# Performance work log

Measured on AMD Instinct MI355X. Metric: run time of the kernel, lower is better.

## Reference

```python
import jax, jax.numpy as jnp
import numpy as np

B, X, H, R, M = 256, 512, 1024, 512, 512
F_BIAS = 1.0

def setup_inputs() -> dict:
    key = jax.random.key(0)
    ks = jax.random.split(key, 8)
    s = lambda fan: 1.0 / np.sqrt(fan)
    return {
        "x": jax.random.normal(ks[0], (B, X), jnp.float32),
        "h": jax.random.normal(ks[1], (B, H), jnp.float32),
        "c": jnp.tanh(jax.random.normal(ks[2], (B, H), jnp.float32)),
        "hmem": jax.random.normal(ks[3], (B, M, R), jnp.float32),
        "W_full": jax.random.normal(ks[4], (X + R + H, R + 4 * H), jnp.float32) * s(X + R + H),
        "bias": jnp.zeros((R + 4 * H,), jnp.float32),
        "W_full1": jax.random.normal(ks[5], (X + R + H, R + H), jnp.float32) * s(X + R + H),
        "bias1": jnp.zeros((R + H,), jnp.float32),
        "trans_w": jax.random.normal(ks[6], (R, X + H), jnp.float32) * s(X + H),
        "trans_b": jnp.zeros((R,), jnp.float32),
        "fc_w": jax.random.normal(ks[7], (M, X + H), jnp.float32) * s(X + H),
        "fc_b": jnp.zeros((M,), jnp.float32),
    }

def reference(x, h, c, hmem, W_full, bias, W_full1, bias1, trans_w, trans_b, fc_w, fc_b):
    h_size = H
    # soft read head over memory slots
    read_head = jnp.concatenate([x, c], axis=1) @ fc_w.T + fc_b          # [B, M]
    h_index = jax.nn.softmax(read_head, axis=1)                          # [B, M]
    h_entry = jnp.einsum('bm,bmr->br', h_index, hmem)                    # [B, R]
    # gated double-projection
    concat = jnp.concatenate([x, c, h_entry], axis=1)                    # [B, X+H+R]
    g = jax.nn.sigmoid(concat @ W_full1 + bias1)                         # [B, R+H]
    gate = jnp.concatenate([jnp.ones_like(x), g], axis=1)                # [B, X+H+R]
    pre = (concat * gate) @ W_full + bias                                # [B, R+4H]
    i = pre[:, 0*h_size:1*h_size]
    j = pre[:, 1*h_size:2*h_size]
    f = pre[:, 2*h_size:3*h_size]
    o = pre[:, 3*h_size:4*h_size]
    om = pre[:, 4*h_size:]                                               # [B, R]
    new_c = jnp.tanh(c * jax.nn.sigmoid(f + F_BIAS) + jax.nn.sigmoid(i) * jnp.tanh(j))
    new_h = new_c * jax.nn.sigmoid(o)
    r_out = h_entry * jax.nn.sigmoid(om)
    # steady-state write: soft index (detached), broadcast overwrite
    w_index = jax.lax.stop_gradient(h_index)                             # [B, M]
    w_val = jnp.concatenate([x, new_c], axis=1) @ trans_w.T + trans_b    # [B, R]
    new_hmem = w_val[:, None, :] * w_index[:, :, None] + hmem * (1.0 - w_index[:, :, None])
    new_r = jnp.concatenate([new_h, r_out], axis=1)                      # [B, H+R]
    return new_r, new_h, new_c, new_hmem
```

## Files before the change

kernel.cpp:

```cpp
#include <hip/hip_runtime.h>
#include <hip/hip_bf16.h>
#include <cstddef>

#define BB 256
#define XX 512
#define HH 1024
#define RR 512
#define MM 512
#define KCAT 2048
#define KXC 1536
#define NFULL 4608
#define NG 1536

#define OFF_NH (BB*1536)
#define OFF_NC (OFF_NH + BB*HH)
#define OFF_HM (OFF_NC + BB*HH)

typedef __attribute__((ext_vector_type(8))) short bf16x8;
typedef __attribute__((ext_vector_type(4))) short s16x4;
typedef __attribute__((ext_vector_type(4))) float f32x4;

__device__ __forceinline__ float sigm(float x) { return 1.0f / (1.0f + expf(-x)); }

__device__ __forceinline__ unsigned short f2bf(float f) {
    unsigned u = __float_as_uint(f);
    u = u + 0x7fffu + ((u >> 16) & 1u);
    return (unsigned short)(u >> 16);
}
__device__ __forceinline__ float bf2f(unsigned short h) {
    return __uint_as_float((unsigned)h << 16);
}


__global__ __launch_bounds__(256) void convw_k(const float* __restrict__ src,
                                               short* __restrict__ hi,
                                               short* __restrict__ lo) {
    size_t e0 = ((size_t)blockIdx.x * 256 + threadIdx.x) * 8;
    short hs[8], ls[8];
    #pragma unroll
    for (int q = 0; q < 2; ++q) {
        float4 v = reinterpret_cast<const float4*>(src + e0)[q];
        float f[4] = {v.x, v.y, v.z, v.w};
        #pragma unroll
        for (int e = 0; e < 4; ++e) {
            unsigned short hb = f2bf(f[e]);
            hs[q * 4 + e] = (short)hb;
            ls[q * 4 + e] = (short)f2bf(f[e] - bf2f(hb));
        }
    }
    *reinterpret_cast<bf16x8*>(hi + e0) = *reinterpret_cast<bf16x8*>(&hs[0]);
    *reinterpret_cast<bf16x8*>(lo + e0) = *reinterpret_cast<bf16x8*>(&ls[0]);
}

__global__ __launch_bounds__(256) void convt_k(const float* __restrict__ W0,
                                               short* __restrict__ T0hi, short* __restrict__ T0lo,
                                               const float* __restrict__ W1,
                                               short* __restrict__ T1hi, short* __restrict__ T1lo) {
    __shared__ __align__(16) short lh[64][72];
    __shared__ __align__(16) short ll[64][72];
    const int tid = threadIdx.x;
    const int by = blockIdx.y;
    const float* W;
    short *Thi, *Tlo;
    int Ndim, n0;
    if (by < 72) { W = W0; Thi = T0hi; Tlo = T0lo; Ndim = NFULL; n0 = by * 64; }
    else         { W = W1; Thi = T1hi; Tlo = T1lo; Ndim = NG;    n0 = (by - 72) * 64; }
    const int k0 = blockIdx.x * 64;
    {
        int kr = (tid >> 4) * 4;
        int nc = (tid & 15) * 4;
        #pragma unroll
        for (int i = 0; i < 4; ++i) {
            float4 v = *reinterpret_cast<const float4*>(W + (size_t)(k0 + kr + i) * Ndim + n0 + nc);
            float f[4] = {v.x, v.y, v.z, v.w};
            #pragma unroll
            for (int e = 0; e < 4; ++e) {
                unsigned short hb = f2bf(f[e]);
                lh[nc + e][kr + i] = (short)hb;
                ll[nc + e][kr + i] = (short)f2bf(f[e] - bf2f(hb));
            }
        }
    }
    __syncthreads();
    {
        int nl = tid >> 2;
        int kq = (tid & 3) * 16;
        size_t base = (size_t)(n0 + nl) * KCAT + k0 + kq;
        *reinterpret_cast<bf16x8*>(Thi + base)     = *reinterpret_cast<const bf16x8*>(&lh[nl][kq]);
        *reinterpret_cast<bf16x8*>(Thi + base + 8) = *reinterpret_cast<const bf16x8*>(&lh[nl][kq + 8]);
        *reinterpret_cast<bf16x8*>(Tlo + base)     = *reinterpret_cast<const bf16x8*>(&ll[nl][kq]);
        *reinterpret_cast<bf16x8*>(Tlo + base + 8) = *reinterpret_cast<const bf16x8*>(&ll[nl][kq + 8]);
    }
}

__global__ __launch_bounds__(256) void prep_k(const float* __restrict__ x,
                                              const float* __restrict__ c,
                                              short* __restrict__ cat_hi,
                                              short* __restrict__ cat_lo) {
    int i = blockIdx.x * 256 + threadIdx.x;
    int e0 = i * 4;
    int b = e0 / KXC, q = e0 - b * KXC;
    float4 v = (q < XX) ? *reinterpret_cast<const float4*>(x + (size_t)b * XX + q)
                        : *reinterpret_cast<const float4*>(c + (size_t)b * HH + (q - XX));
    float f[4] = {v.x, v.y, v.z, v.w};
    s16x4 hv, lv;
    #pragma unroll
    for (int e = 0; e < 4; ++e) {
        unsigned short hb = f2bf(f[e]);
        hv[e] = (short)hb;
        lv[e] = (short)f2bf(f[e] - bf2f(hb));
    }
    *reinterpret_cast<s16x4*>(cat_hi + (size_t)b * KCAT + q) = hv;
    *reinterpret_cast<s16x4*>(cat_lo + (size_t)b * KCAT + q) = lv;
}

template<int GATHER>
__global__ __launch_bounds__(256, 2) void mgemm_k(const short* __restrict__ A0h,
                                                  const short* __restrict__ A0l, int lda0,
                                                  const short* __restrict__ A1h,
                                                  const short* __restrict__ A1l, int lda1,
                                                  const short* __restrict__ Bh_,
                                                  const short* __restrict__ Bl_, int ldb,
                                                  const float* __restrict__ bias,
                                                  float* __restrict__ Cbase, int ldc,
                                                  size_t chunk_stride, int kchunk) {
    __shared__ __align__(16) short Ah[64][72];
    __shared__ __align__(16) short Al[64][72];
    __shared__ __align__(16) short Bh[128][72];
    __shared__ __align__(16) short Bl[128][72];

    const int tid = threadIdx.x;
    const int col0 = blockIdx.x * 128;
    const int row0 = blockIdx.y * 64;
    const int z = blockIdx.z;
    const int kbeg = z * kchunk;
    float* C = Cbase + (size_t)z * chunk_stride;

    const int lane = tid & 63, w = tid >> 6;
    const int rm = (w >> 1) * 32, cn = (w & 1) * 64;
    const int fr = lane & 15, kg = lane >> 4;

    const int ar = tid >> 2, akq = (tid & 3) * 16;
    const int br = tid >> 1, bkq = (tid & 1) * 32;

    f32x4 acc[2][4] = {};
    int4 pa[4], pb[8];

    const short* bHrow = Bh_ + (size_t)(col0 + br) * ldb + bkq;
    const short* bLrow = Bl_ + (size_t)(col0 + br) * ldb + bkq;

    const int steps = kchunk >> 6;

    {
        int gk = kbeg + akq;
        const short* ah_ = (GATHER && gk >= XX) ? A1h + (size_t)(row0 + ar) * lda1 + (gk - XX)
                                                : A0h + (size_t)(row0 + ar) * lda0 + gk;
        const short* al_ = (GATHER && gk >= XX) ? A1l + (size_t)(row0 + ar) * lda1 + (gk - XX)
                                                : A0l + (size_t)(row0 + ar) * lda0 + gk;
        pa[0] = *reinterpret_cast<const int4*>(ah_);
        pa[1] = *reinterpret_cast<const int4*>(ah_ + 8);
        pa[2] = *reinterpret_cast<const int4*>(al_);
        pa[3] = *reinterpret_cast<const int4*>(al_ + 8);
        #pragma unroll
        for (int j = 0; j < 4; ++j) {
            pb[j]     = *reinterpret_cast<const int4*>(bHrow + kbeg + j * 8);
            pb[4 + j] = *reinterpret_cast<const int4*>(bLrow + kbeg + j * 8);
        }
    }

    for (int t = 0; t < steps; ++t) {
        *reinterpret_cast<int4*>(&Ah[ar][akq])     = pa[0];
        *reinterpret_cast<int4*>(&Ah[ar][akq + 8]) = pa[1];
        *reinterpret_cast<int4*>(&Al[ar][akq])     = pa[2];
        *reinterpret_cast<int4*>(&Al[ar][akq + 8]) = pa[3];
        #pragma unroll
        for (int j = 0; j < 4; ++j) {
            *reinterpret_cast<int4*>(&Bh[br][bkq + j * 8]) = pb[j];
            *reinterpret_cast<int4*>(&Bl[br][bkq + j * 8]) = pb[4 + j];
        }
        __syncthreads();
        if (t + 1 < steps) {
            int kc = kbeg + (t + 1) * 64;
            int gk = kc + akq;
            const short* ah_ = (GATHER && gk >= XX) ? A1h + (size_t)(row0 + ar) * lda1 + (gk - XX)
                                                    : A0h + (size_t)(row0 + ar) * lda0 + gk;
            const short* al_ = (GATHER && gk >= XX) ? A1l + (size_t)(row0 + ar) * lda1 + (gk - XX)
                                                    : A0l + (size_t)(row0 + ar) * lda0 + gk;
            pa[0] = *reinterpret_cast<const int4*>(ah_);
            pa[1] = *reinterpret_cast<const int4*>(ah_ + 8);
            pa[2] = *reinterpret_cast<const int4*>(al_);
            pa[3] = *reinterpret_cast<const int4*>(al_ + 8);
            #pragma unroll
            for (int j = 0; j < 4; ++j) {
                pb[j]     = *reinterpret_cast<const int4*>(bHrow + kc + j * 8);
                pb[4 + j] = *reinterpret_cast<const int4*>(bLrow + kc + j * 8);
            }
        }
        #pragma unroll
        for (int ks = 0; ks < 64; ks += 32) {
            bf16x8 ah2[2], al2[2], bh4[4], bl4[4];
            #pragma unroll
            for (int mf = 0; mf < 2; ++mf) {
                ah2[mf] = *reinterpret_cast<const bf16x8*>(&Ah[rm + mf * 16 + fr][ks + kg * 8]);
                al2[mf] = *reinterpret_cast<const bf16x8*>(&Al[rm + mf * 16 + fr][ks + kg * 8]);
            }
            #pragma unroll
            for (int nf = 0; nf < 4; ++nf) {
                bh4[nf] = *reinterpret_cast<const bf16x8*>(&Bh[cn + nf * 16 + fr][ks + kg * 8]);
                bl4[nf] = *reinterpret_cast<const bf16x8*>(&Bl[cn + nf * 16 + fr][ks + kg * 8]);
            }
            #pragma unroll
            for (int mf = 0; mf < 2; ++mf)
                #pragma unroll
                for (int nf = 0; nf < 4; ++nf) {
                    acc[mf][nf] = __builtin_amdgcn_mfma_f32_16x16x32_bf16(ah2[mf], bh4[nf], acc[mf][nf], 0, 0, 0);
                    acc[mf][nf] = __builtin_amdgcn_mfma_f32_16x16x32_bf16(ah2[mf], bl4[nf], acc[mf][nf], 0, 0, 0);
                    acc[mf][nf] = __builtin_amdgcn_mfma_f32_16x16x32_bf16(al2[mf], bh4[nf], acc[mf][nf], 0, 0, 0);
                }
        }
        __syncthreads();
    }

    #pragma unroll
    for (int mf = 0; mf < 2; ++mf)
        #pragma unroll
        for (int nf = 0; nf < 4; ++nf)
            #pragma unroll
            for (int i = 0; i < 4; ++i) {
                int row = row0 + rm + mf * 16 + kg * 4 + i;
                int col = col0 + cn + nf * 16 + fr;
                float v = acc[mf][nf][i];
                if (z == 0) v += bias[col];
                C[(size_t)row * ldc + col] = v;
            }
}

__global__ __launch_bounds__(512) void smax_k(const float* __restrict__ rhp,
                                              float* __restrict__ hidx) {
    __shared__ float red[8];
    __shared__ float red2[8];
    int b = blockIdx.x, t = threadIdx.x;
    float v = 0.f;
    #pragma unroll
    for (int zz = 0; zz < 6; ++zz) v += rhp[(size_t)zz * (BB * MM) + (size_t)b * MM + t];
    float m = v;
    #pragma unroll
    for (int off = 1; off < 64; off <<= 1) m = fmaxf(m, __shfl_xor(m, off));
    int wid = t >> 6, lane = t & 63;
    if (lane == 0) red[wid] = m;
    __syncthreads();
    float mm = red[0];
    #pragma unroll
    for (int i = 1; i < 8; ++i) mm = fmaxf(mm, red[i]);
    float e = expf(v - mm);
    float s = e;
    #pragma unroll
    for (int off = 1; off < 64; off <<= 1) s += __shfl_xor(s, off);
    if (lane == 0) red2[wid] = s;
    __syncthreads();
    float tot = red2[0];
    #pragma unroll
    for (int i = 1; i < 8; ++i) tot += red2[i];
    hidx[(size_t)b * MM + t] = e / tot;
}

__global__ __launch_bounds__(512) void hepart_k(const float* __restrict__ hidx,
                                                const float* __restrict__ hmem,
                                                float* __restrict__ hep) {
    __shared__ float wi[128];
    int b = blockIdx.x, s = blockIdx.y, t = threadIdx.x;
    if (t < 128) wi[t] = hidx[(size_t)b * MM + s * 128 + t];
    __syncthreads();
    const float* hm = hmem + ((size_t)b * MM + (size_t)s * 128) * RR + t;
    float acc = 0.f;
    #pragma unroll 8
    for (int j = 0; j < 128; ++j) acc += wi[j] * hm[(size_t)j * RR];
    hep[((size_t)s * BB + b) * RR + t] = acc;
}

__global__ __launch_bounds__(256) void hefin_k(const float* __restrict__ hep,
                                               short* __restrict__ cat_hi,
                                               short* __restrict__ cat_lo) {
    int i = blockIdx.x * 256 + threadIdx.x;
    int b = i >> 9, r = i & (RR - 1);
    float acc = 0.f;
    #pragma unroll
    for (int s = 0; s < 4; ++s) acc += hep[((size_t)s * BB + b) * RR + r];
    size_t base = (size_t)b * KCAT + KXC + r;
    unsigned short hb = f2bf(acc);
    cat_hi[base] = (short)hb;
    cat_lo[base] = (short)f2bf(acc - bf2f(hb));
}

__global__ __launch_bounds__(256) void gfin_k(const float* __restrict__ gp,
                                              const short* __restrict__ cat_hi,
                                              const short* __restrict__ cat_lo,
                                              short* __restrict__ gatg_hi,
                                              short* __restrict__ gatg_lo) {
    int i = blockIdx.x * 256 + threadIdx.x;
    int b = i / NG, q = i - b * NG;
    float s = 0.f;
    #pragma unroll
    for (int zz = 0; zz < 4; ++zz) s += gp[(size_t)zz * (BB * NG) + (size_t)b * NG + q];
    size_t base = (size_t)b * KCAT + XX + q;
    float e = bf2f((unsigned short)cat_hi[base]) + bf2f((unsigned short)cat_lo[base]);
    float gv = e * sigm(s);
    unsigned short hb = f2bf(gv);
    gatg_hi[(size_t)b * NG + q] = (short)hb;
    gatg_lo[(size_t)b * NG + q] = (short)f2bf(gv - bf2f(hb));
}

__global__ __launch_bounds__(256) void lstm_k(const float* __restrict__ pre0,
                                              const float* __restrict__ c,
                                              const short* __restrict__ cat_hi,
                                              const short* __restrict__ cat_lo,
                                              float* __restrict__ out,
                                              short* __restrict__ ncg_hi,
                                              short* __restrict__ ncg_lo) {
    const float* pre1 = pre0 + (size_t)BB * NFULL;
    int idx = blockIdx.x * 256 + threadIdx.x;
    int b = idx / 1536, q = idx - b * 1536;
    size_t pb = (size_t)b * NFULL;
    if (q < HH) {
        float iv = pre0[pb + q] + pre1[pb + q];
        float jv = pre0[pb + HH + q] + pre1[pb + HH + q];
        float fv = pre0[pb + 2 * HH + q] + pre1[pb + 2 * HH + q];
        float ov = pre0[pb + 3 * HH + q] + pre1[pb + 3 * HH + q];
        float cc = c[(size_t)b * HH + q];
        float nc = tanhf(cc * sigm(fv + 1.0f) + sigm(iv) * tanhf(jv));
        float nh = nc * sigm(ov);
        out[(size_t)b * 1536 + q] = nh;
        out[OFF_NH + (size_t)b * HH + q] = nh;
        out[OFF_NC + (size_t)b * HH + q] = nc;
        unsigned short hb = f2bf(nc);
        ncg_hi[(size_t)b * HH + q] = (short)hb;
        ncg_lo[(size_t)b * HH + q] = (short)f2bf(nc - bf2f(hb));
    } else {
        int r = q - HH;
        float om = pre0[pb + 4 * HH + r] + pre1[pb + 4 * HH + r];
        size_t base = (size_t)b * KCAT + KXC + r;
        float he = bf2f((unsigned short)cat_hi[base]) + bf2f((unsigned short)cat_lo[base]);
        out[(size_t)b * 1536 + HH + r] = he * sigm(om);
    }
}

__global__ __launch_bounds__(256) void wvred_k(const float* __restrict__ wvp,
                                               float* __restrict__ wval) {
    int i = blockIdx.x * 256 + threadIdx.x;
    size_t e = (size_t)i * 4;
    float4 acc = {0.f, 0.f, 0.f, 0.f};
    #pragma unroll
    for (int zz = 0; zz < 6; ++zz) {
        float4 p = *reinterpret_cast<const float4*>(wvp + (size_t)zz * (BB * RR) + e);
        acc.x += p.x; acc.y += p.y; acc.z += p.z; acc.w += p.w;
    }
    *reinterpret_cast<float4*>(wval + e) = acc;
}

__global__ __launch_bounds__(256) void hmemupd_k(const float* __restrict__ hmem,
                                                 const float* __restrict__ wval,
                                                 const float* __restrict__ widx,
                                                 float* __restrict__ outhm) {
    size_t n4 = (size_t)BB * MM * RR / 4;
    size_t stride = (size_t)gridDim.x * blockDim.x;
    for (size_t i = (size_t)blockIdx.x * blockDim.x + threadIdx.x; i < n4; i += stride) {
        size_t e = i * 4;
        int r = (int)(e & (RR - 1));
        int m = (int)((e >> 9) & (MM - 1));
        int b = (int)(e >> 18);
        float wi = widx[(size_t)b * MM + m];
        float om = 1.0f - wi;
        float4 hv = *reinterpret_cast<const float4*>(hmem + e);
        float4 wv = *reinterpret_cast<const float4*>(wval + (size_t)b * RR + r);
        float4 o;
        o.x = wv.x * wi + hv.x * om;
        o.y = wv.y * wi + hv.y * om;
        o.z = wv.z * wi + hv.z * om;
        o.w = wv.w * wi + hv.w * om;
        *reinterpret_cast<float4*>(outhm + e) = o;
    }
}


__global__ __launch_bounds__(256) void prep3_k(const float* __restrict__ x,
                                               const float* __restrict__ c,
                                               float* __restrict__ concatb,
                                               float* __restrict__ gated) {
    int idx = blockIdx.x * 256 + threadIdx.x;
    int b = idx / KXC, q = idx - b * KXC;
    float v;
    if (q < XX) { v = x[b * XX + q]; gated[(size_t)b * KCAT + q] = v; }
    else v = c[b * HH + (q - XX)];
    concatb[(size_t)b * KCAT + q] = v;
}

template<int AMODE, int BLAYOUT, int EPI>
__global__ __launch_bounds__(256) void mgemm3_k(const float* __restrict__ A0,
                                                const float* __restrict__ A1,
                                                const float* __restrict__ W,
                                                const float* __restrict__ bias,
                                                float* __restrict__ C,
                                                const float* __restrict__ E,
                                                int N, int K) {
    __shared__ __align__(16) short Ah[64][72];
    __shared__ __align__(16) short Al[64][72];
    __shared__ __align__(16) short Bh[64][72];
    __shared__ __align__(16) short Bl[64][72];
    const int tid = threadIdx.x;
    const int row0 = blockIdx.y * 64, col0 = blockIdx.x * 64;
    const int lane = tid & 63, w = tid >> 6;
    const int rm = (w >> 1) * 32, cn = (w & 1) * 32;
    const int fr = lane & 15, kg = lane >> 4;
    const int ar = tid >> 2, akq = (tid & 3) * 16;
    const int bkk = (tid >> 4) * 4, bnn = (tid & 15) * 4;
    f32x4 acc[2][2] = {};
    for (int k0 = 0; k0 < K; k0 += 64) {
        {
            const float* src;
            if (AMODE == 0) src = A0 + (size_t)(row0 + ar) * K + k0 + akq;
            else {
                int gk = k0 + akq;
                src = (gk < XX) ? (A0 + (size_t)(row0 + ar) * XX + gk)
                                : (A1 + (size_t)(row0 + ar) * HH + (gk - XX));
            }
            short hs[16], ls[16];
            #pragma unroll
            for (int q = 0; q < 4; ++q) {
                float4 v = reinterpret_cast<const float4*>(src)[q];
                float f[4] = {v.x, v.y, v.z, v.w};
                #pragma unroll
                for (int e = 0; e < 4; ++e) {
                    unsigned short hb = f2bf(f[e]);
                    hs[q * 4 + e] = (short)hb;
                    ls[q * 4 + e] = (short)f2bf(f[e] - bf2f(hb));
                }
            }
            *reinterpret_cast<bf16x8*>(&Ah[ar][akq])     = *reinterpret_cast<bf16x8*>(&hs[0]);
            *reinterpret_cast<bf16x8*>(&Ah[ar][akq + 8]) = *reinterpret_cast<bf16x8*>(&hs[8]);
            *reinterpret_cast<bf16x8*>(&Al[ar][akq])     = *reinterpret_cast<bf16x8*>(&ls[0]);
            *reinterpret_cast<bf16x8*>(&Al[ar][akq + 8]) = *reinterpret_cast<bf16x8*>(&ls[8]);
        }
        if (BLAYOUT == 1) {
            const float* src = W + (size_t)(col0 + ar) * K + k0 + akq;
            short hs[16], ls[16];
            #pragma unroll
            for (int q = 0; q < 4; ++q) {
                float4 v = reinterpret_cast<const float4*>(src)[q];
                float f[4] = {v.x, v.y, v.z, v.w};
                #pragma unroll
                for (int e = 0; e < 4; ++e) {
                    unsigned short hb = f2bf(f[e]);
                    hs[q * 4 + e] = (short)hb;
                    ls[q * 4 + e] = (short)f2bf(f[e] - bf2f(hb));
                }
            }
            *reinterpret_cast<bf16x8*>(&Bh[ar][akq])     = *reinterpret_cast<bf16x8*>(&hs[0]);
            *reinterpret_cast<bf16x8*>(&Bh[ar][akq + 8]) = *reinterpret_cast<bf16x8*>(&hs[8]);
            *reinterpret_cast<bf16x8*>(&Bl[ar][akq])     = *reinterpret_cast<bf16x8*>(&ls[0]);
            *reinterpret_cast<bf16x8*>(&Bl[ar][akq + 8]) = *reinterpret_cast<bf16x8*>(&ls[8]);
        } else {
            float4 r0 = *reinterpret_cast<const float4*>(W + (size_t)(k0 + bkk + 0) * N + col0 + bnn);
            float4 r1 = *reinterpret_cast<const float4*>(W + (size_t)(k0 + bkk + 1) * N + col0 + bnn);
            float4 r2 = *reinterpret_cast<const float4*>(W + (size_t)(k0 + bkk + 2) * N + col0 + bnn);
            float4 r3 = *reinterpret_cast<const float4*>(W + (size_t)(k0 + bkk + 3) * N + col0 + bnn);
            float col[4][4] = {{r0.x, r1.x, r2.x, r3.x}, {r0.y, r1.y, r2.y, r3.y},
                               {r0.z, r1.z, r2.z, r3.z}, {r0.w, r1.w, r2.w, r3.w}};
            #pragma unroll
            for (int j = 0; j < 4; ++j) {
                s16x4 hv, lv;
                #pragma unroll
                for (int e = 0; e < 4; ++e) {
                    unsigned short hb = f2bf(col[j][e]);
                    hv[e] = (short)hb;
                    lv[e] = (short)f2bf(col[j][e] - bf2f(hb));
                }
                *reinterpret_cast<s16x4*>(&Bh[bnn + j][bkk]) = hv;
                *reinterpret_cast<s16x4*>(&Bl[bnn + j][bkk]) = lv;
            }
        }
        __syncthreads();
        #pragma unroll
        for (int ks = 0; ks < 64; ks += 32) {
            bf16x8 ah[2], al[2], bh[2], bl[2];
            #pragma unroll
            for (int mf = 0; mf < 2; ++mf) {
                ah[mf] = *reinterpret_cast<const bf16x8*>(&Ah[rm + mf * 16 + fr][ks + kg * 8]);
                al[mf] = *reinterpret_cast<const bf16x8*>(&Al[rm + mf * 16 + fr][ks + kg * 8]);
            }
            #pragma unroll
            for (int nf = 0; nf < 2; ++nf) {
                bh[nf] = *reinterpret_cast<const bf16x8*>(&Bh[cn + nf * 16 + fr][ks + kg * 8]);
                bl[nf] = *reinterpret_cast<const bf16x8*>(&Bl[cn + nf * 16 + fr][ks + kg * 8]);
            }
            #pragma unroll
            for (int mf = 0; mf < 2; ++mf)
                #pragma unroll
                for (int nf = 0; nf < 2; ++nf) {
                    acc[mf][nf] = __builtin_amdgcn_mfma_f32_16x16x32_bf16(ah[mf], bh[nf], acc[mf][nf], 0, 0, 0);
                    acc[mf][nf] = __builtin_amdgcn_mfma_f32_16x16x32_bf16(ah[mf], bl[nf], acc[mf][nf], 0, 0, 0);
                    acc[mf][nf] = __builtin_amdgcn_mfma_f32_16x16x32_bf16(al[mf], bh[nf], acc[mf][nf], 0, 0, 0);
                }
        }
        __syncthreads();
    }
    #pragma unroll
    for (int mf = 0; mf < 2; ++mf)
        #pragma unroll
        for (int nf = 0; nf < 2; ++nf)
            #pragma unroll
            for (int i = 0; i < 4; ++i) {
                int row = row0 + rm + mf * 16 + kg * 4 + i;
                int col = col0 + cn + nf * 16 + fr;
                float v = acc[mf][nf][i] + bias[col];
                if (EPI == 0) C[(size_t)row * N + col] = v;
                else {
                    size_t base = (size_t)row * KCAT + XX + col;
                    C[base] = E[base] * sigm(v);
                }
            }
}

__global__ __launch_bounds__(256) void softmax3_k(float* __restrict__ rh) {
    int b = blockIdx.x;
    float* row = rh + (size_t)b * MM;
    int t = threadIdx.x;
    float v0 = row[t], v1 = row[t + 256];
    float m = fmaxf(v0, v1);
    #pragma unroll
    for (int off = 1; off < 64; off <<= 1) m = fmaxf(m, __shfl_xor(m, off));
    __shared__ float red[8];
    int wid = t >> 6, lane = t & 63;
    if (lane == 0) red[wid] = m;
    __syncthreads();
    float mm = fmaxf(fmaxf(red[0], red[1]), fmaxf(red[2], red[3]));
    float e0 = expf(v0 - mm), e1 = expf(v1 - mm);
    float s = e0 + e1;
    #pragma unroll
    for (int off = 1; off < 64; off <<= 1) s += __shfl_xor(s, off);
    if (lane == 0) red[4 + wid] = s;
    __syncthreads();
    float inv = 1.0f / (red[4] + red[5] + red[6] + red[7]);
    row[t] = e0 * inv;
    row[t + 256] = e1 * inv;
}

__global__ __launch_bounds__(512) void hentry3_k(const float* __restrict__ hidx,
                                                 const float* __restrict__ hmem,
                                                 float* __restrict__ concatb) {
    int b = blockIdx.x;
    int r = threadIdx.x;
    __shared__ float wi[MM];
    wi[r] = hidx[(size_t)b * MM + r];
    __syncthreads();
    const float* hm = hmem + (size_t)b * MM * RR + r;
    float acc = 0.f;
    #pragma unroll 8
    for (int m = 0; m < MM; ++m) acc += wi[m] * hm[(size_t)m * RR];
    concatb[(size_t)b * KCAT + KXC + r] = acc;
}

__global__ __launch_bounds__(256) void lstm3_k(const float* __restrict__ pre,
                                               const float* __restrict__ c,
                                               const float* __restrict__ concatb,
                                               float* __restrict__ out) {
    int idx = blockIdx.x * 256 + threadIdx.x;
    int b = idx / 1536, q = idx - b * 1536;
    const float* p = pre + (size_t)b * NFULL;
    if (q < HH) {
        float iv = p[q], jv = p[HH + q], fv = p[2 * HH + q], ov = p[3 * HH + q];
        float cc = c[(size_t)b * HH + q];
        float nc = tanhf(cc * sigm(fv + 1.0f) + sigm(iv) * tanhf(jv));
        float nh = nc * sigm(ov);
        out[(size_t)b * 1536 + q] = nh;
        out[OFF_NH + (size_t)b * HH + q] = nh;
        out[OFF_NC + (size_t)b * HH + q] = nc;
    } else {
        int r = q - HH;
        float om = p[4 * HH + r];
        float he = concatb[(size_t)b * KCAT + KXC + r];
        out[(size_t)b * 1536 + HH + r] = he * sigm(om);
    }
}

extern "C" void kernel_launch(void* const* d_in, const int* in_sizes, int n_in,
                              void* d_out, int out_size, void* d_ws, size_t ws_size,
                              hipStream_t stream) {
    const float* x      = (const float*)d_in[0];
    const float* c      = (const float*)d_in[2];
    const float* hmem   = (const float*)d_in[3];
    const float* W_full = (const float*)d_in[4];
    const float* bias   = (const float*)d_in[5];
    const float* W_full1= (const float*)d_in[6];
    const float* bias1  = (const float*)d_in[7];
    const float* trans_w= (const float*)d_in[8];
    const float* trans_b= (const float*)d_in[9];
    const float* fc_w   = (const float*)d_in[10];
    const float* fc_b   = (const float*)d_in[11];

    float* out = (float*)d_out;

    constexpr size_t SZ_WT    = (size_t)NFULL * KCAT * 2;
    constexpr size_t SZ_WT1   = (size_t)NG * KCAT * 2;
    constexpr size_t SZ_FCW   = (size_t)MM * KXC * 2;
    constexpr size_t SZ_CAT   = (size_t)BB * KCAT * 2;
    constexpr size_t SZ_GATG  = (size_t)BB * NG * 2;
    constexpr size_t SZ_NCG   = (size_t)BB * HH * 2;
    constexpr size_t SZ_HIDX  = (size_t)BB * MM * 4;
    constexpr size_t SZ_RH6   = 6 * (size_t)BB * MM * 4;
    constexpr size_t SZ_HEP   = 4 * (size_t)BB * RR * 4;
    constexpr size_t SZ_GP4   = 4 * (size_t)BB * NG * 4;
    constexpr size_t SZ_PRE2  = 2 * (size_t)BB * NFULL * 4;
    constexpr size_t SZ_WV6   = 6 * (size_t)BB * RR * 4;
    constexpr size_t SZ_WVAL  = (size_t)BB * RR * 4;
    constexpr size_t SZ_WT1R  = 2 * SZ_WT1;
    constexpr size_t SZ_FWR   = 2 * SZ_FCW;
    constexpr size_t SZ_G1    = SZ_PRE2;
    constexpr size_t NEED = 2 * SZ_WT + SZ_WT1R + SZ_FWR + 2 * SZ_CAT
                          + 2 * SZ_GATG + 2 * SZ_NCG + SZ_HIDX + SZ_G1;

    if (ws_size >= NEED) {
        char* p = (char*)d_ws;
        short* wt_hi   = (short*)p; p += SZ_WT;
        short* wt_lo   = (short*)p; p += SZ_WT;
        char*  wt1r    = p;         p += SZ_WT1R;
        char*  fwr     = p;         p += SZ_FWR;
        short* cat_hi  = (short*)p; p += SZ_CAT;
        short* cat_lo  = (short*)p; p += SZ_CAT;
        short* gatg_hi = (short*)p; p += SZ_GATG;
        short* gatg_lo = (short*)p; p += SZ_GATG;
        short* ncg_hi  = (short*)p; p += SZ_NCG;
        short* ncg_lo  = (short*)p; p += SZ_NCG;
        float* hidx    = (float*)p; p += SZ_HIDX;
        char*  g1      = p;

        short* wt1_hi = (short*)wt1r;
        short* wt1_lo = (short*)(wt1r + SZ_WT1);
        float* wv6    = (float*)wt1r;
        float* wval   = (float*)(wt1r + SZ_WV6);
        short* fcw_hi = (short*)fwr;
        short* fcw_lo = (short*)(fwr + SZ_FCW);
        short* trw_hi = (short*)fwr;
        short* trw_lo = (short*)(fwr + SZ_FCW);
        float* rh6    = (float*)g1;
        float* hep    = (float*)g1;
        float* gp4    = (float*)g1;
        float* pre2   = (float*)g1;

        convt_k<<<dim3(KCAT / 64, 96), 256, 0, stream>>>(W_full, wt_hi, wt_lo,
                                                         W_full1, wt1_hi, wt1_lo);
        convw_k<<<MM * KXC / 8 / 256, 256, 0, stream>>>(fc_w, fcw_hi, fcw_lo);
        prep_k<<<BB * KXC / 4 / 256, 256, 0, stream>>>(x, c, cat_hi, cat_lo);
        mgemm_k<0><<<dim3(MM / 128, BB / 64, 6), 256, 0, stream>>>(
            cat_hi, cat_lo, KCAT, nullptr, nullptr, 0,
            fcw_hi, fcw_lo, KXC, fc_b, rh6, MM, (size_t)BB * MM, KXC / 6);
        smax_k<<<BB, 512, 0, stream>>>(rh6, hidx);
        hepart_k<<<dim3(BB, 4), 512, 0, stream>>>(hidx, hmem, hep);
        hefin_k<<<BB * RR / 256, 256, 0, stream>>>(hep, cat_hi, cat_lo);
        mgemm_k<0><<<dim3(NG / 128, BB / 64, 4), 256, 0, stream>>>(
            cat_hi, cat_lo, KCAT, nullptr, nullptr, 0,
            wt1_hi, wt1_lo, KCAT, bias1, gp4, NG, (size_t)BB * NG, KCAT / 4);
        gfin_k<<<BB * NG / 256, 256, 0, stream>>>(gp4, cat_hi, cat_lo, gatg_hi, gatg_lo);
        mgemm_k<1><<<dim3(NFULL / 128, BB / 64, 2), 256, 0, stream>>>(
            cat_hi, cat_lo, KCAT, gatg_hi, gatg_lo, NG,
            wt_hi, wt_lo, KCAT, bias, pre2, NFULL, (size_t)BB * NFULL, KCAT / 2);
        lstm_k<<<BB * 1536 / 256, 256, 0, stream>>>(pre2, c, cat_hi, cat_lo,
                                                    out, ncg_hi, ncg_lo);
        convw_k<<<RR * KXC / 8 / 256, 256, 0, stream>>>(trans_w, trw_hi, trw_lo);
        mgemm_k<1><<<dim3(RR / 128, BB / 64, 6), 256, 0, stream>>>(
            cat_hi, cat_lo, KCAT, ncg_hi, ncg_lo, HH,
            trw_hi, trw_lo, KXC, trans_b, wv6, RR, (size_t)BB * RR, KXC / 6);
        wvred_k<<<BB * RR / 4 / 256, 256, 0, stream>>>(wv6, wval);
        hmemupd_k<<<4096, 256, 0, stream>>>(hmem, wval, hidx, out + OFF_HM);
    } else {
        float* ws      = (float*)d_ws;
        float* hidx    = ws;
        float* concatb = hidx + BB * MM;
        float* gated   = concatb + BB * KCAT;
        float* pre     = gated + BB * KCAT;
        float* wval    = pre + BB * NFULL;
        float* new_c   = out + OFF_NC;

        prep3_k<<<BB * KXC / 256, 256, 0, stream>>>(x, c, concatb, gated);
        mgemm3_k<1, 1, 0><<<dim3(MM / 64, BB / 64), 256, 0, stream>>>(
            x, c, fc_w, fc_b, hidx, nullptr, MM, KXC);
        softmax3_k<<<BB, 256, 0, stream>>>(hidx);
        hentry3_k<<<BB, 512, 0, stream>>>(hidx, hmem, concatb);
        mgemm3_k<0, 0, 1><<<dim3(NG / 64, BB / 64), 256, 0, stream>>>(
            concatb, nullptr, W_full1, bias1, gated, concatb, NG, KCAT);
        mgemm3_k<0, 0, 0><<<dim3(NFULL / 64, BB / 64), 256, 0, stream>>>(
            gated, nullptr, W_full, bias, pre, nullptr, NFULL, KCAT);
        lstm3_k<<<BB * 1536 / 256, 256, 0, stream>>>(pre, c, concatb, out);
        mgemm3_k<1, 1, 0><<<dim3(RR / 64, BB / 64), 256, 0, stream>>>(
            x, new_c, trans_w, trans_b, wval, nullptr, RR, KXC);
        hmemupd_k<<<4096, 256, 0, stream>>>(hmem, wval, hidx, out + OFF_HM);
    }
}
```

Baseline: 402.0 us.

## Enlarge GEMM tiles to 128x128 with swizzled LDS and fuse partial reduction into hmem update

The split-bf16 MFMA GEMM now uses 128x128 output tiles, with each wave computing a 64x64 sub-tile. Shared memory is unpadded and XOR-swizzled to avoid bank conflicts, and the K-split count for the narrow GEMMs is doubled to 12 to keep enough blocks. The separate wvred reduction kernel is removed, and the hmem update kernel now sums the 12 partials per batch row in shared memory before streaming the memory update. The larger tiles raise reuse per LDS load but cut the block count and raise register pressure. The extra K-splits also mean more partial traffic.

```diff
diff --git a/kernel.cpp b/kernel.cpp
--- a/kernel.cpp
+++ b/kernel.cpp
@@ -124,105 +124,116 @@
                                                   const float* __restrict__ bias,
                                                   float* __restrict__ Cbase, int ldc,
                                                   size_t chunk_stride, int kchunk) {
-    __shared__ __align__(16) short Ah[64][72];
-    __shared__ __align__(16) short Al[64][72];
-    __shared__ __align__(16) short Bh[128][72];
-    __shared__ __align__(16) short Bl[128][72];
+    __shared__ __align__(16) short Ah[128 * 64];
+    __shared__ __align__(16) short Al[128 * 64];
+    __shared__ __align__(16) short Bh[128 * 64];
+    __shared__ __align__(16) short Bl[128 * 64];
 
     const int tid = threadIdx.x;
-    const int col0 = blockIdx.x * 128;
-    const int row0 = blockIdx.y * 64;
+    const int col0 = blockIdx.x * 128, row0 = blockIdx.y * 128;
     const int z = blockIdx.z;
     const int kbeg = z * kchunk;
     float* C = Cbase + (size_t)z * chunk_stride;
 
     const int lane = tid & 63, w = tid >> 6;
-    const int rm = (w >> 1) * 32, cn = (w & 1) * 64;
+    const int rm = (w >> 1) * 64, cn = (w & 1) * 64;
     const int fr = lane & 15, kg = lane >> 4;
 
-    const int ar = tid >> 2, akq = (tid & 3) * 16;
-    const int br = tid >> 1, bkq = (tid & 1) * 32;
-
-    f32x4 acc[2][4] = {};
-    int4 pa[4], pb[8];
-
-    const short* bHrow = Bh_ + (size_t)(col0 + br) * ldb + bkq;
-    const short* bLrow = Bl_ + (size_t)(col0 + br) * ldb + bkq;
+    const int sr = tid >> 1;
+    const int so = (tid & 1) * 64;
+    const int sks = so >> 1;
+    const int swr = (sr & 7) << 4;
+
+    f32x4 acc[4][4] = {};
+    int4 pa[8], pb[8];
 
     const int steps = kchunk >> 6;
 
-    {
-        int gk = kbeg + akq;
-        const short* ah_ = (GATHER && gk >= XX) ? A1h + (size_t)(row0 + ar) * lda1 + (gk - XX)
-                                                : A0h + (size_t)(row0 + ar) * lda0 + gk;
-        const short* al_ = (GATHER && gk >= XX) ? A1l + (size_t)(row0 + ar) * lda1 + (gk - XX)
-                                                : A0l + (size_t)(row0 + ar) * lda0 + gk;
-        pa[0] = *reinterpret_cast<const int4*>(ah_);
-        pa[1] = *reinterpret_cast<const int4*>(ah_ + 8);
-        pa[2] = *reinterpret_cast<const int4*>(al_);
-        pa[3] = *reinterpret_cast<const int4*>(al_ + 8);
+    #define LOADA(GK0)                                                           \
+        {   int gk = (GK0) + sks;                                                \
+            const short *ah_, *al_;                                              \
+            if (GATHER && gk >= XX) {                                            \
+                ah_ = A1h + (size_t)(row0 + sr) * lda1 + (gk - XX);              \
+                al_ = A1l + (size_t)(row0 + sr) * lda1 + (gk - XX);              \
+            } else {                                                             \
+                ah_ = A0h + (size_t)(row0 + sr) * lda0 + gk;                     \
+                al_ = A0l + (size_t)(row0 + sr) * lda0 + gk;                     \
+            }                                                                    \
+            pa[0] = *reinterpret_cast<const int4*>(ah_);                         \
+            pa[1] = *reinterpret_cast<const int4*>(ah_ + 8);                     \
+            pa[2] = *reinterpret_cast<const int4*>(ah_ + 16);                    \
+            pa[3] = *reinterpret_cast<const int4*>(ah_ + 24);                    \
+            pa[4] = *reinterpret_cast<const int4*>(al_);                         \
+            pa[5] = *reinterpret_cast<const int4*>(al_ + 8);                     \
+            pa[6] = *reinterpret_cast<const int4*>(al_ + 16);                    \
+            pa[7] = *reinterpret_cast<const int4*>(al_ + 24);                    \
+        }
+    #define LOADB(GK0)                                                           \
+        {   const short* bh_ = Bh_ + (size_t)(col0 + sr) * ldb + (GK0) + sks;    \
+            const short* bl_ = Bl_ + (size_t)(col0 + sr) * ldb + (GK0) + sks;    \
+            pb[0] = *reinterpret_cast<const int4*>(bh_);                         \
+            pb[1] = *reinterpret_cast<const int4*>(bh_ + 8);                     \
+            pb[2] = *reinterpret_cast<const int4*>(bh_ + 16);                    \
+            pb[3] = *reinterpret_cast<const int4*>(bh_ + 24);                    \
+            pb[4] = *reinterpret_cast<const int4*>(bl_);                         \
+            pb[5] = *reinterpret_cast<const int4*>(bl_ + 8);                     \
+            pb[6] = *reinterpret_cast<const int4*>(bl_ + 16);                    \
+            pb[7] = *reinterpret_cast<const int4*>(bl_ + 24);                    \
+        }
+
+    LOADA(kbeg)
+    LOADB(kbeg)
+
+    char* aH = (char*)Ah + sr * 128;
+    char* aL = (char*)Al + sr * 128;
+    char* bH = (char*)Bh + sr * 128;
+    char* bL = (char*)Bl + sr * 128;
+
+    for (int t = 0; t < steps; ++t) {
         #pragma unroll
         for (int j = 0; j < 4; ++j) {
-            pb[j]     = *reinterpret_cast<const int4*>(bHrow + kbeg + j * 8);
-            pb[4 + j] = *reinterpret_cast<const int4*>(bLrow + kbeg + j * 8);
-        }
-    }
-
-    for (int t = 0; t < steps; ++t) {
-        *reinterpret_cast<int4*>(&Ah[ar][akq])     = pa[0];
-        *reinterpret_cast<int4*>(&Ah[ar][akq + 8]) = pa[1];
-        *reinterpret_cast<int4*>(&Al[ar][akq])     = pa[2];
-        *reinterpret_cast<int4*>(&Al[ar][akq + 8]) = pa[3];
-        #pragma unroll
-        for (int j = 0; j < 4; ++j) {
-            *reinterpret_cast<int4*>(&Bh[br][bkq + j * 8]) = pb[j];
-            *reinterpret_cast<int4*>(&Bl[br][bkq + j * 8]) = pb[4 + j];
+            int off = (so + j * 16) ^ swr;
+            *reinterpret_cast<int4*>(aH + off) = pa[j];
+            *reinterpret_cast<int4*>(aL + off) = pa[4 + j];
+            *reinterpret_cast<int4*>(bH + off) = pb[j];
+            *reinterpret_cast<int4*>(bL + off) = pb[4 + j];
         }
         __syncthreads();
         if (t + 1 < steps) {
             int kc = kbeg + (t + 1) * 64;
-            int gk = kc + akq;
-            const short* ah_ = (GATHER && gk >= XX) ? A1h + (size_t)(row0 + ar) * lda1 + (gk - XX)
-                                                    : A0h + (size_t)(row0 + ar) * lda0 + gk;
-            const short* al_ = (GATHER && gk >= XX) ? A1l + (size_t)(row0 + ar) * lda1 + (gk - XX)
-                                                    : A0l + (size_t)(row0 + ar) * lda0 + gk;
-            pa[0] = *reinterpret_cast<const int4*>(ah_);
-            pa[1] = *reinterpret_cast<const int4*>(ah_ + 8);
-            pa[2] = *reinterpret_cast<const int4*>(al_);
-            pa[3] = *reinterpret_cast<const int4*>(al_ + 8);
-            #pragma unroll
-            for (int j = 0; j < 4; ++j) {
-                pb[j]     = *reinterpret_cast<const int4*>(bHrow + kc + j * 8);
-                pb[4 + j] = *reinterpret_cast<const int4*>(bLrow + kc + j * 8);
-            }
+            LOADA(kc)
+            LOADB(kc)
         }
         #pragma unroll
-        for (int ks = 0; ks < 64; ks += 32) {
-            bf16x8 ah2[2], al2[2], bh4[4], bl4[4];
-            #pragma unroll
-            for (int mf = 0; mf < 2; ++mf) {
-                ah2[mf] = *reinterpret_cast<const bf16x8*>(&Ah[rm + mf * 16 + fr][ks + kg * 8]);
-                al2[mf] = *reinterpret_cast<const bf16x8*>(&Al[rm + mf * 16 + fr][ks + kg * 8]);
+        for (int ksi = 0; ksi < 2; ++ksi) {
+            int fro = (ksi * 64 + kg * 16) ^ ((fr & 7) << 4);
+            bf16x8 ah4[4], al4[4];
+            #pragma unroll
+            for (int mf = 0; mf < 4; ++mf) {
+                int row = rm + mf * 16 + fr;
+                ah4[mf] = *reinterpret_cast<const bf16x8*>((char*)Ah + row * 128 + fro);
+                al4[mf] = *reinterpret_cast<const bf16x8*>((char*)Al + row * 128 + fro);
             }
             #pragma unroll
             for (int nf = 0; nf < 4; ++nf) {
-                bh4[nf] = *reinterpret_cast<const bf16x8*>(&Bh[cn + nf * 16 + fr][ks + kg * 8]);
-                bl4[nf] = *reinterpret_cast<const bf16x8*>(&Bl[cn + nf * 16 + fr][ks + kg * 8]);
-            }
-            #pragma unroll
-            for (int mf = 0; mf < 2; ++mf)
+                int col = cn + nf * 16 + fr;
+                bf16x8 bh8 = *reinterpret_cast<const bf16x8*>((char*)Bh + col * 128 + fro);
+                bf16x8 bl8 = *reinterpret_cast<const bf16x8*>((char*)Bl + col * 128 + fro);
                 #pragma unroll
-                for (int nf = 0; nf < 4; ++nf) {
-                    acc[mf][nf] = __builtin_amdgcn_mfma_f32_16x16x32_bf16(ah2[mf], bh4[nf], acc[mf][nf], 0, 0, 0);
-                    acc[mf][nf] = __builtin_amdgcn_mfma_f32_16x16x32_bf16(ah2[mf], bl4[nf], acc[mf][nf], 0, 0, 0);
-                    acc[mf][nf] = __builtin_amdgcn_mfma_f32_16x16x32_bf16(al2[mf], bh4[nf], acc[mf][nf], 0, 0, 0);
+                for (int mf = 0; mf < 4; ++mf) {
+                    acc[mf][nf] = __builtin_amdgcn_mfma_f32_16x16x32_bf16(ah4[mf], bh8, acc[mf][nf], 0, 0, 0);
+                    acc[mf][nf] = __builtin_amdgcn_mfma_f32_16x16x32_bf16(ah4[mf], bl8, acc[mf][nf], 0, 0, 0);
+                    acc[mf][nf] = __builtin_amdgcn_mfma_f32_16x16x32_bf16(al4[mf], bh8, acc[mf][nf], 0, 0, 0);
                 }
+            }
         }
         __syncthreads();
     }
-
-    #pragma unroll
-    for (int mf = 0; mf < 2; ++mf)
+    #undef LOADA
+    #undef LOADB
+
+    #pragma unroll
+    for (int mf = 0; mf < 4; ++mf)
         #pragma unroll
         for (int nf = 0; nf < 4; ++nf)
             #pragma unroll
@@ -242,7 +253,7 @@
     int b = blockIdx.x, t = threadIdx.x;
     float v = 0.f;
     #pragma unroll
-    for (int zz = 0; zz < 6; ++zz) v += rhp[(size_t)zz * (BB * MM) + (size_t)b * MM + t];
+    for (int zz = 0; zz < 12; ++zz) v += rhp[(size_t)zz * (BB * MM) + (size_t)b * MM + t];
     float m = v;
     #pragma unroll
     for (int off = 1; off < 64; off <<= 1) m = fmaxf(m, __shfl_xor(m, off));
@@ -344,39 +355,40 @@
     }
 }
 
-__global__ __launch_bounds__(256) void wvred_k(const float* __restrict__ wvp,
-                                               float* __restrict__ wval) {
-    int i = blockIdx.x * 256 + threadIdx.x;
-    size_t e = (size_t)i * 4;
-    float4 acc = {0.f, 0.f, 0.f, 0.f};
-    #pragma unroll
-    for (int zz = 0; zz < 6; ++zz) {
-        float4 p = *reinterpret_cast<const float4*>(wvp + (size_t)zz * (BB * RR) + e);
-        acc.x += p.x; acc.y += p.y; acc.z += p.z; acc.w += p.w;
-    }
-    *reinterpret_cast<float4*>(wval + e) = acc;
-}
-
 __global__ __launch_bounds__(256) void hmemupd_k(const float* __restrict__ hmem,
-                                                 const float* __restrict__ wval,
+                                                 const float* __restrict__ wvp,
                                                  const float* __restrict__ widx,
                                                  float* __restrict__ outhm) {
-    size_t n4 = (size_t)BB * MM * RR / 4;
-    size_t stride = (size_t)gridDim.x * blockDim.x;
-    for (size_t i = (size_t)blockIdx.x * blockDim.x + threadIdx.x; i < n4; i += stride) {
-        size_t e = i * 4;
-        int r = (int)(e & (RR - 1));
-        int m = (int)((e >> 9) & (MM - 1));
-        int b = (int)(e >> 18);
-        float wi = widx[(size_t)b * MM + m];
-        float om = 1.0f - wi;
+    __shared__ float wv[RR];
+    __shared__ float wi[256];
+    int b = blockIdx.x, half = blockIdx.y, t = threadIdx.x;
+    #pragma unroll
+    for (int j = 0; j < 2; ++j) {
+        int r = t + j * 256;
+        float s = 0.f;
+        #pragma unroll
+        for (int zz = 0; zz < 12; ++zz)
+            s += wvp[(size_t)zz * (BB * RR) + (size_t)b * RR + r];
+        wv[r] = s;
+    }
+    wi[t] = widx[(size_t)b * MM + half * 256 + t];
+    __syncthreads();
+    int r4 = t & 127;
+    int mo = t >> 7;
+    size_t base = ((size_t)b * MM + (size_t)half * 256) * RR + (size_t)r4 * 4;
+    float4 wv4 = *reinterpret_cast<const float4*>(&wv[r4 * 4]);
+    #pragma unroll 4
+    for (int it = 0; it < 128; ++it) {
+        int m = it * 2 + mo;
+        float w = wi[m];
+        float omw = 1.0f - w;
+        size_t e = base + (size_t)m * RR;
         float4 hv = *reinterpret_cast<const float4*>(hmem + e);
-        float4 wv = *reinterpret_cast<const float4*>(wval + (size_t)b * RR + r);
         float4 o;
-        o.x = wv.x * wi + hv.x * om;
-        o.y = wv.y * wi + hv.y * om;
-        o.z = wv.z * wi + hv.z * om;
-        o.w = wv.w * wi + hv.w * om;
+        o.x = wv4.x * w + hv.x * omw;
+        o.y = wv4.y * w + hv.y * omw;
+        o.z = wv4.z * w + hv.z * omw;
+        o.w = wv4.w * w + hv.w * omw;
         *reinterpret_cast<float4*>(outhm + e) = o;
     }
 }
@@ -582,6 +594,30 @@
     }
 }
 
+__global__ __launch_bounds__(256) void hmemupd3_k(const float* __restrict__ hmem,
+                                                  const float* __restrict__ wval,
+                                                  const float* __restrict__ widx,
+                                                  float* __restrict__ outhm) {
+    size_t n4 = (size_t)BB * MM * RR / 4;
+    size_t stride = (size_t)gridDim.x * blockDim.x;
+    for (size_t i = (size_t)blockIdx.x * blockDim.x + threadIdx.x; i < n4; i += stride) {
+        size_t e = i * 4;
+        int r = (int)(e & (RR - 1));
+        int m = (int)((e >> 9) & (MM - 1));
+        int b = (int)(e >> 18);
+        float wi = widx[(size_t)b * MM + m];
+        float om = 1.0f - wi;
+        float4 hv = *reinterpret_cast<const float4*>(hmem + e);
+        float4 wv = *reinterpret_cast<const float4*>(wval + (size_t)b * RR + r);
+        float4 o;
+        o.x = wv.x * wi + hv.x * om;
+        o.y = wv.y * wi + hv.y * om;
+        o.z = wv.z * wi + hv.z * om;
+        o.w = wv.w * wi + hv.w * om;
+        *reinterpret_cast<float4*>(outhm + e) = o;
+    }
+}
+
 extern "C" void kernel_launch(void* const* d_in, const int* in_sizes, int n_in,
                               void* d_out, int out_size, void* d_ws, size_t ws_size,
                               hipStream_t stream) {
@@ -606,12 +642,7 @@
     constexpr size_t SZ_GATG  = (size_t)BB * NG * 2;
     constexpr size_t SZ_NCG   = (size_t)BB * HH * 2;
     constexpr size_t SZ_HIDX  = (size_t)BB * MM * 4;
-    constexpr size_t SZ_RH6   = 6 * (size_t)BB * MM * 4;
-    constexpr size_t SZ_HEP   = 4 * (size_t)BB * RR * 4;
-    constexpr size_t SZ_GP4   = 4 * (size_t)BB * NG * 4;
     constexpr size_t SZ_PRE2  = 2 * (size_t)BB * NFULL * 4;
-    constexpr size_t SZ_WV6   = 6 * (size_t)BB * RR * 4;
-    constexpr size_t SZ_WVAL  = (size_t)BB * RR * 4;
     constexpr size_t SZ_WT1R  = 2 * SZ_WT1;
     constexpr size_t SZ_FWR   = 2 * SZ_FCW;
     constexpr size_t SZ_G1    = SZ_PRE2;
@@ -635,13 +666,12 @@
 
         short* wt1_hi = (short*)wt1r;
         short* wt1_lo = (short*)(wt1r + SZ_WT1);
-        float* wv6    = (float*)wt1r;
-        float* wval   = (float*)(wt1r + SZ_WV6);
+        float* wv12   = (float*)wt1r;
         short* fcw_hi = (short*)fwr;
         short* fcw_lo = (short*)(fwr + SZ_FCW);
         short* trw_hi = (short*)fwr;
         short* trw_lo = (short*)(fwr + SZ_FCW);
-        float* rh6    = (float*)g1;
+        float* rh12   = (float*)g1;
         float* hep    = (float*)g1;
         float* gp4    = (float*)g1;
         float* pre2   = (float*)g1;
@@ -650,27 +680,26 @@
                                                          W_full1, wt1_hi, wt1_lo);
         convw_k<<<MM * KXC / 8 / 256, 256, 0, stream>>>(fc_w, fcw_hi, fcw_lo);
         prep_k<<<BB * KXC / 4 / 256, 256, 0, stream>>>(x, c, cat_hi, cat_lo);
-        mgemm_k<0><<<dim3(MM / 128, BB / 64, 6), 256, 0, stream>>>(
+        mgemm_k<0><<<dim3(MM / 128, BB / 128, 12), 256, 0, stream>>>(
             cat_hi, cat_lo, KCAT, nullptr, nullptr, 0,
-            fcw_hi, fcw_lo, KXC, fc_b, rh6, MM, (size_t)BB * MM, KXC / 6);
-        smax_k<<<BB, 512, 0, stream>>>(rh6, hidx);
+            fcw_hi, fcw_lo, KXC, fc_b, rh12, MM, (size_t)BB * MM, KXC / 12);
+        smax_k<<<BB, 512, 0, stream>>>(rh12, hidx);
         hepart_k<<<dim3(BB, 4), 512, 0, stream>>>(hidx, hmem, hep);
         hefin_k<<<BB * RR / 256, 256, 0, stream>>>(hep, cat_hi, cat_lo);
-        mgemm_k<0><<<dim3(NG / 128, BB / 64, 4), 256, 0, stream>>>(
+        mgemm_k<0><<<dim3(NG / 128, BB / 128, 4), 256, 0, stream>>>(
             cat_hi, cat_lo, KCAT, nullptr, nullptr, 0,
             wt1_hi, wt1_lo, KCAT, bias1, gp4, NG, (size_t)BB * NG, KCAT / 4);
         gfin_k<<<BB * NG / 256, 256, 0, stream>>>(gp4, cat_hi, cat_lo, gatg_hi, gatg_lo);
-        mgemm_k<1><<<dim3(NFULL / 128, BB / 64, 2), 256, 0, stream>>>(
+        mgemm_k<1><<<dim3(NFULL / 128, BB / 128, 2), 256, 0, stream>>>(
             cat_hi, cat_lo, KCAT, gatg_hi, gatg_lo, NG,
             wt_hi, wt_lo, KCAT, bias, pre2, NFULL, (size_t)BB * NFULL, KCAT / 2);
         lstm_k<<<BB * 1536 / 256, 256, 0, stream>>>(pre2, c, cat_hi, cat_lo,
                                                     out, ncg_hi, ncg_lo);
         convw_k<<<RR * KXC / 8 / 256, 256, 0, stream>>>(trans_w, trw_hi, trw_lo);
-        mgemm_k<1><<<dim3(RR / 128, BB / 64, 6), 256, 0, stream>>>(
+        mgemm_k<1><<<dim3(RR / 128, BB / 128, 12), 256, 0, stream>>>(
             cat_hi, cat_lo, KCAT, ncg_hi, ncg_lo, HH,
-            trw_hi, trw_lo, KXC, trans_b, wv6, RR, (size_t)BB * RR, KXC / 6);
-        wvred_k<<<BB * RR / 4 / 256, 256, 0, stream>>>(wv6, wval);
-        hmemupd_k<<<4096, 256, 0, stream>>>(hmem, wval, hidx, out + OFF_HM);
+            trw_hi, trw_lo, KXC, trans_b, wv12, RR, (size_t)BB * RR, KXC / 12);
+        hmemupd_k<<<dim3(BB, 2), 256, 0, stream>>>(hmem, wv12, hidx, out + OFF_HM);
     } else {
         float* ws      = (float*)d_ws;
         float* hidx    = ws;
@@ -692,6 +721,6 @@
         lstm3_k<<<BB * 1536 / 256, 256, 0, stream>>>(pre, c, concatb, out);
         mgemm3_k<1, 1, 0><<<dim3(RR / 64, BB / 64), 256, 0, stream>>>(
             x, new_c, trans_w, trans_b, wval, nullptr, RR, KXC);
-        hmemupd_k<<<4096, 256, 0, stream>>>(hmem, wval, hidx, out + OFF_HM);
-    }
-}
+        hmemupd3_k<<<4096, 256, 0, stream>>>(hmem, wval, hidx, out + OFF_HM);
+    }
+}
```

New measurement: 449.6 us. +11.8%, slower.
